# Kernel optimization log

Hardware: AMD Instinct MI355X
Metric: run time of the kernel (lower is better)

Reference implementation:

```python
import jax, jax.numpy as jnp
import numpy as np

SIG_LEVEL = 2
N_UNITS = 1024
INPUT_SIZE = 512
SIGSIZE = sum(2 ** k for k in range(1, SIG_LEVEL + 1))  # siglength(2, L) = 2^(L+1)-2 = 6
SAVED_LEN = N_UNITS * (1 + SIGSIZE)  # 7168
BATCH = 4096


def sigjoin(prev_sigs, disp, time_lapse, level):
    """Chen's identity: new_sig = prev_sig (tensor-mult) exp(v), truncated at `level`.

    prev_sigs: [N, SIGSIZE] flat signature levels (level k occupies 2^k entries),
    disp: [N, 1] displacement in dim 0; dim 1 displacement fixed to time_lapse.
    """
    N = prev_sigs.shape[0]
    v = jnp.concatenate([disp, jnp.full_like(disp, 1.0) * time_lapse], axis=1)  # [N, 2]
    # signature of the straight segment: seg_k = v^{(x)k} / k!
    seg = [v]
    for k in range(2, level + 1):
        seg.append((seg[-1][:, :, None] * v[:, None, :]).reshape(N, -1) / k)
    # split prev signature into levels
    S, off = [], 0
    for k in range(1, level + 1):
        sz = 2 ** k
        S.append(prev_sigs[:, off:off + sz])
        off += sz
    # result_k = S_k + seg_k + sum_{i=1}^{k-1} S_i (x) seg_{k-i}
    out = []
    for k in range(1, level + 1):
        r = S[k - 1] + seg[k - 1]
        for i in range(1, k):
            r = r + (S[i - 1][:, :, None] * seg[k - i - 1][:, None, :]).reshape(N, 2 ** k)
        out.append(r)
    return jnp.concatenate(out, axis=1)


def setup_inputs() -> dict:
    key = jax.random.key(0)
    ks = jax.random.split(key, 8)
    x = jax.random.normal(ks[0], (BATCH, INPUT_SIZE), dtype=jnp.float32)
    prev_sigs = jax.random.normal(ks[1], (BATCH, N_UNITS * SIGSIZE), dtype=jnp.float32) * 0.1
    prev_states = jax.random.normal(ks[2], (BATCH, N_UNITS), dtype=jnp.float32)
    W_w = jax.random.normal(ks[3], (N_UNITS, INPUT_SIZE), dtype=jnp.float32) / np.sqrt(INPUT_SIZE)
    W_b = jax.random.normal(ks[4], (N_UNITS,), dtype=jnp.float32) * 0.01
    U_w = jax.random.normal(ks[5], (N_UNITS, SAVED_LEN), dtype=jnp.float32) / np.sqrt(SAVED_LEN)
    U_b = jax.random.normal(ks[6], (N_UNITS,), dtype=jnp.float32) * 0.01
    log_timelapse = jnp.array([np.log(0.1)], dtype=jnp.float32)
    return {"x": x, "prev_sigs": prev_sigs, "prev_states": prev_states,
            "W_w": W_w, "W_b": W_b, "U_w": U_w, "U_b": U_b,
            "log_timelapse": log_timelapse}


def reference(x, prev_sigs, prev_states, W_w, W_b, U_w, U_b, log_timelapse):
    h = x @ W_w.T + W_b                                  # [B, n_units]
    mem = jnp.concatenate([prev_sigs, prev_states], 1)   # [B, saved_len]
    raw = h + mem @ U_w.T + U_b                          # [B, n_units]
    disp = (raw - prev_states).reshape(-1, 1)            # [B*n_units, 1]
    tl = jnp.exp(log_timelapse)[0]
    sigs = sigjoin(prev_sigs.reshape(-1, SIGSIZE), disp, tl, SIG_LEVEL)
    sigs = sigs.reshape(-1, N_UNITS * SIGSIZE)
    # output_signatures=True: output = [sigs, raw_output]
    return jnp.concatenate([sigs, raw], axis=1)          # [B, n_units*(sigsize+1)]
```

## Files before the change

kernel.cpp:

```cpp
#include <hip/hip_runtime.h>
#include <hip/hip_bf16.h>
#include <cmath>

#define BATCH   4096
#define NUNITS  1024
#define INSIZE  512
#define SIGSZ   6
#define KSIG    (NUNITS * SIGSZ)
#define SAVED   (KSIG + NUNITS)
#define KTOT    (INSIZE + KSIG + NUNITS)
#define OUTW    (NUNITS * (SIGSZ + 1))
#define NKT     (KTOT / 64)

#define WS_AX 0LL
#define WS_AS 2097152LL
#define WS_AT 27262976LL
#define WS_BW 31457280LL
#define WS_BU 31981568LL
#define WS_ELEMS 39321600LL
#define WS_BYTES (WS_ELEMS * 2)

typedef __attribute__((ext_vector_type(8))) short bf16x8;
typedef __attribute__((ext_vector_type(8))) unsigned short u16x8;
typedef __attribute__((ext_vector_type(4))) float f32x4;

__device__ __forceinline__ unsigned short f2bf(float f) {
    union { float f; unsigned int u; } c; c.f = f;
    unsigned int u = c.u;
    return (unsigned short)((u + 0x7FFFu + ((u >> 16) & 1u)) >> 16);
}
__device__ __forceinline__ float bf2f(unsigned short h) {
    union { unsigned int u; float f; } c; c.u = ((unsigned int)h) << 16;
    return c.f;
}

__device__ __forceinline__ int swz(int row, int bytecol) {
    return row * 64 + (((bytecol) ^ ((row & 7) << 4)) >> 1);
}

__global__ __launch_bounds__(256)
void prepack(const float* __restrict__ x, const float* __restrict__ sigs,
             const float* __restrict__ states, const float* __restrict__ Ww,
             const float* __restrict__ Uw, unsigned short* __restrict__ ws)
{
    const long long stride = (long long)gridDim.x * blockDim.x;
    for (long long p = (long long)blockIdx.x * blockDim.x + threadIdx.x;
         p < 4915200LL; p += stride) {
        const float* src; unsigned short* dst; long long o;
        if (p < 262144LL)       { src = x;      dst = ws + WS_AX; o = p; }
        else if (p < 3407872LL) { src = sigs;   dst = ws + WS_AS; o = p - 262144LL; }
        else if (p < 3932160LL) { src = states; dst = ws + WS_AT; o = p - 3407872LL; }
        else if (p < 3997696LL) { src = Ww;     dst = ws + WS_BW; o = p - 3932160LL; }
        else                    { src = Uw;     dst = ws + WS_BU; o = p - 3997696LL; }
        const f32x4 v0 = __builtin_nontemporal_load((const f32x4*)(src + o * 8));
        const f32x4 v1 = __builtin_nontemporal_load((const f32x4*)(src + o * 8) + 1);
        u16x8 h;
        h[0] = f2bf(v0[0]); h[1] = f2bf(v0[1]); h[2] = f2bf(v0[2]); h[3] = f2bf(v0[3]);
        h[4] = f2bf(v1[0]); h[5] = f2bf(v1[1]); h[6] = f2bf(v1[2]); h[7] = f2bf(v1[3]);
        *(u16x8*)(dst + o * 8) = h;
    }
}

#define GLD_LDS(G, L) __builtin_amdgcn_global_load_lds(                        \
        (const __attribute__((address_space(1))) unsigned int*)(G),           \
        (__attribute__((address_space(3))) unsigned int*)(L), 16, 0, 0)

__global__ __launch_bounds__(1024, 1)
void rsig_gemm(const unsigned short* __restrict__ ws,
               const float* __restrict__ Wb,
               const float* __restrict__ Ub,
               const float* __restrict__ lt,
               float* __restrict__ out)
{
    __shared__ unsigned short lds[3 * 16384 + 16384];

    const int t  = threadIdx.x;
    const int bn = blockIdx.x & 7;
    const int bm = blockIdx.x >> 3;

    const int lane = t & 63;
    const int w    = t >> 6;
    const int wm   = w >> 3;
    const int wn   = (w >> 1) & 3;
    const int wk   = w & 1;
    const int lr   = lane & 15;
    const int lg   = lane >> 4;

    const unsigned short* wsAx = ws + WS_AX;
    const unsigned short* wsAs = ws + WS_AS;
    const unsigned short* wsAt = ws + WS_AT;
    const unsigned short* wsBw = ws + WS_BW;
    const unsigned short* wsBu = ws + WS_BU;

    unsigned short* stash = &lds[3 * 16384];
    const int kt0 = 104 + bn * 2;

    const int sRow = lane >> 3;
    const int sCol = 8 * ((lane & 7) ^ sRow);
    const int arow = bm * 128 + w * 8 + sRow;
    const int brow = bn * 128 + w * 8 + sRow;

    f32x4 acc[4][2];
#pragma unroll
    for (int m = 0; m < 4; ++m)
#pragma unroll
        for (int n = 0; n < 2; ++n)
            acc[m][n] = (f32x4)0.f;

    {
        const unsigned short* ga = wsAx + (size_t)arow * INSIZE + sCol;
        const unsigned short* gb = wsBw + (size_t)brow * INSIZE + sCol;
        GLD_LDS(ga,       &lds[0 * 16384 + w * 512]);
        GLD_LDS(gb,       &lds[0 * 16384 + 8192 + w * 512]);
        GLD_LDS(ga + 64,  &lds[1 * 16384 + w * 512]);
        GLD_LDS(gb + 64,  &lds[1 * 16384 + 8192 + w * 512]);
    }

    const unsigned short* saPtr = wsAx + (size_t)arow * INSIZE + 128 + sCol;
    const unsigned short* sbPtr = wsBw + (size_t)brow * INSIZE + 128 + sCol;

    int cur = 0;
    for (int kt = 0; kt < NKT; ++kt) {
        if (kt < NKT - 1) { asm volatile("s_waitcnt vmcnt(2)" ::: "memory"); }
        else              { asm volatile("s_waitcnt vmcnt(0)" ::: "memory"); }
        __builtin_amdgcn_s_barrier();
        __builtin_amdgcn_sched_barrier(0);

        const int st = kt + 2;
        if (st < NKT) {
            if (st == 8) {
                saPtr = wsAs + (size_t)arow * KSIG  + sCol;
                sbPtr = wsBu + (size_t)brow * SAVED + sCol;
            } else if (st == 104) {
                saPtr = wsAt + (size_t)arow * NUNITS + sCol;
            }
            int nb = cur + 2; if (nb >= 3) nb -= 3;
            unsigned short* base = &lds[nb * 16384];
            GLD_LDS(saPtr, base + w * 512);
            GLD_LDS(sbPtr, base + 8192 + w * 512);
            saPtr += 64;
            sbPtr += 64;
        }

        if (kt == kt0) {
            const u16x8 v = *(const u16x8*)&lds[cur * 16384 + t * 8];
            *(u16x8*)&stash[t * 8] = v;
        } else if (kt == kt0 + 1) {
            const u16x8 v = *(const u16x8*)&lds[cur * 16384 + t * 8];
            *(u16x8*)&stash[8192 + t * 8] = v;
        }

        {
            const unsigned short* aT = &lds[cur * 16384];
            const unsigned short* bT = aT + 8192;
            bf16x8 af[4], bfr[2];
#pragma unroll
            for (int m = 0; m < 4; ++m)
                af[m] = *(const bf16x8*)&aT[swz(wm * 64 + m * 16 + lr, wk * 64 + lg * 16)];
#pragma unroll
            for (int n = 0; n < 2; ++n)
                bfr[n] = *(const bf16x8*)&bT[swz(wn * 32 + n * 16 + lr, wk * 64 + lg * 16)];
            __builtin_amdgcn_s_setprio(1);
#pragma unroll
            for (int m = 0; m < 4; ++m)
#pragma unroll
                for (int n = 0; n < 2; ++n)
                    acc[m][n] = __builtin_amdgcn_mfma_f32_16x16x32_bf16(af[m], bfr[n], acc[m][n], 0, 0, 0);
            __builtin_amdgcn_s_setprio(0);
        }

        cur = (cur == 2) ? 0 : cur + 1;
    }

    __syncthreads();

    float* rawt = (float*)lds;
    if (wk == 0) {
#pragma unroll
        for (int n = 0; n < 2; ++n) {
            const int cc = wn * 32 + n * 16 + lr;
            const int ug = bn * 128 + cc;
            const float bias = Wb[ug] + Ub[ug];
#pragma unroll
            for (int m = 0; m < 4; ++m) {
                const int rr = wm * 64 + m * 16 + lg * 4;
#pragma unroll
                for (int i = 0; i < 4; ++i)
                    rawt[(rr + i) * 132 + cc] = acc[m][n][i] + bias;
            }
        }
    }
    __syncthreads();
    if (wk == 1) {
#pragma unroll
        for (int n = 0; n < 2; ++n) {
            const int cc = wn * 32 + n * 16 + lr;
#pragma unroll
            for (int m = 0; m < 4; ++m) {
                const int rr = wm * 64 + m * 16 + lg * 4;
#pragma unroll
                for (int i = 0; i < 4; ++i)
                    rawt[(rr + i) * 132 + cc] += acc[m][n][i];
            }
        }
    }
    __syncthreads();

    const float tl = expf(lt[0]);
    const int r0 = t >> 8;
    const int c  = t & 255;

#define PS(R, CC) bf2f(stash[((CC) >> 6) * 8192 + ((R) >> 3) * 512 + ((R) & 7) * 64 \
                            + (((((CC) & 63) >> 3) ^ ((R) & 7)) << 3) + ((CC) & 7)])

    for (int pass = 0; pass < 32; ++pass) {
        const int r = pass * 4 + r0;
        const long long b = (long long)bm * 128 + r;
        if (c < 192) {
            const int u  = (2 * c) / 3;
            const int cs = c % 3;
            const unsigned short* srow = wsAs + b * KSIG + bn * 768;
            const ushort4 sin = *(const ushort4*)(srow + c * 4);
            const float e0 = bf2f(sin.x), e1 = bf2f(sin.y);
            const float e2 = bf2f(sin.z), e3 = bf2f(sin.w);
            float4 o;
            if (cs == 0) {
                const float d = rawt[r * 132 + u] - PS(r, u);
                o.x = e0 + d;
                o.y = e1 + tl;
                o.z = e2 + d  * (0.5f * d  + e0);
                o.w = e3 + tl * (0.5f * d  + e0);
            } else if (cs == 1) {
                const float d  = rawt[r * 132 + u]     - PS(r, u);
                const float dn = rawt[r * 132 + u + 1] - PS(r, u + 1);
                const float s1 = bf2f(srow[u * 6 + 1]);
                o.x = e0 + d  * (0.5f * tl + s1);
                o.y = e1 + tl * (0.5f * tl + s1);
                o.z = e2 + dn;
                o.w = e3 + tl;
            } else {
                const float d = rawt[r * 132 + u] - PS(r, u);
                const unsigned int sv = *(const unsigned int*)(srow + u * 6);
                const float s0 = bf2f((unsigned short)(sv & 0xffffu));
                const float s1 = bf2f((unsigned short)(sv >> 16));
                o.x = e0 + d  * (0.5f * d  + s0);
                o.y = e1 + tl * (0.5f * d  + s0);
                o.z = e2 + d  * (0.5f * tl + s1);
                o.w = e3 + tl * (0.5f * tl + s1);
            }
            *(float4*)(out + b * OUTW + bn * 768 + c * 4) = o;
        } else if (c < 224) {
            const int cc = (c - 192) * 4;
            const float4 rv = *(const float4*)&rawt[r * 132 + cc];
            *(float4*)(out + b * OUTW + KSIG + bn * 128 + cc) = rv;
        }
    }
#undef PS
}

extern "C" void kernel_launch(void* const* d_in, const int* in_sizes, int n_in,
                              void* d_out, int out_size, void* d_ws, size_t ws_size,
                              hipStream_t stream) {
    const float* x      = (const float*)d_in[0];
    const float* sigs   = (const float*)d_in[1];
    const float* states = (const float*)d_in[2];
    const float* Ww     = (const float*)d_in[3];
    const float* Wb     = (const float*)d_in[4];
    const float* Uw     = (const float*)d_in[5];
    const float* Ub     = (const float*)d_in[6];
    const float* lt     = (const float*)d_in[7];
    float* out = (float*)d_out;

    unsigned short* ws = (unsigned short*)d_ws;
    hipLaunchKernelGGL(prepack, dim3(2048), dim3(256), 0, stream,
                       x, sigs, states, Ww, Uw, ws);
    hipLaunchKernelGGL(rsig_gemm, dim3(256), dim3(1024), 0, stream,
                       ws, Wb, Ub, lt, out);
}
```

Before: 147.5 us.

## Switch GEMM to 32x32x16 MFMA with four-way K split across waves

Replaces the 16x16x32 bf16 MFMA tiling with 32x32x16 MFMA, re-partitioning the 16 waves into 2 M by 2 N by 4 K groups with 64x64 per-wave tiles. This is meant to cut LDS fragment reads per MFMA and raise MFMA efficiency. The cost is a four-stage serialized split-K reduction through LDS with extra barriers in the epilogue. The s_setprio hints are also dropped.

```diff
diff --git a/kernel.cpp b/kernel.cpp
--- a/kernel.cpp
+++ b/kernel.cpp
@@ -20,9 +20,10 @@
 #define WS_ELEMS 39321600LL
 #define WS_BYTES (WS_ELEMS * 2)
 
-typedef __attribute__((ext_vector_type(8))) short bf16x8;
-typedef __attribute__((ext_vector_type(8))) unsigned short u16x8;
-typedef __attribute__((ext_vector_type(4))) float f32x4;
+typedef __attribute__((ext_vector_type(8)))  short bf16x8;
+typedef __attribute__((ext_vector_type(8)))  unsigned short u16x8;
+typedef __attribute__((ext_vector_type(4)))  float f32x4;
+typedef __attribute__((ext_vector_type(16))) float f32x16;
 
 __device__ __forceinline__ unsigned short f2bf(float f) {
     union { float f; unsigned int u; } c; c.f = f;
@@ -81,10 +82,11 @@
     const int lane = t & 63;
     const int w    = t >> 6;
     const int wm   = w >> 3;
-    const int wn   = (w >> 1) & 3;
-    const int wk   = w & 1;
-    const int lr   = lane & 15;
-    const int lg   = lane >> 4;
+    const int wn   = (w >> 2) & 1;
+    const int wk   = w & 3;
+    const int l31  = lane & 31;
+    const int lkh  = lane >> 5;
+    const int rcol = wk * 32 + lkh * 16;
 
     const unsigned short* wsAx = ws + WS_AX;
     const unsigned short* wsAs = ws + WS_AS;
@@ -100,12 +102,12 @@
     const int arow = bm * 128 + w * 8 + sRow;
     const int brow = bn * 128 + w * 8 + sRow;
 
-    f32x4 acc[4][2];
-#pragma unroll
-    for (int m = 0; m < 4; ++m)
+    f32x16 acc[2][2];
+#pragma unroll
+    for (int m = 0; m < 2; ++m)
 #pragma unroll
         for (int n = 0; n < 2; ++n)
-            acc[m][n] = (f32x4)0.f;
+            acc[m][n] = (f32x16)0.f;
 
     {
         const unsigned short* ga = wsAx + (size_t)arow * INSIZE + sCol;
@@ -153,20 +155,19 @@
         {
             const unsigned short* aT = &lds[cur * 16384];
             const unsigned short* bT = aT + 8192;
-            bf16x8 af[4], bfr[2];
-#pragma unroll
-            for (int m = 0; m < 4; ++m)
-                af[m] = *(const bf16x8*)&aT[swz(wm * 64 + m * 16 + lr, wk * 64 + lg * 16)];
+            bf16x8 af[2], bfr[2];
+#pragma unroll
+            for (int m = 0; m < 2; ++m)
+                af[m] = *(const bf16x8*)&aT[swz(wm * 64 + m * 32 + l31, rcol)];
 #pragma unroll
             for (int n = 0; n < 2; ++n)
-                bfr[n] = *(const bf16x8*)&bT[swz(wn * 32 + n * 16 + lr, wk * 64 + lg * 16)];
-            __builtin_amdgcn_s_setprio(1);
-#pragma unroll
-            for (int m = 0; m < 4; ++m)
+                bfr[n] = *(const bf16x8*)&bT[swz(wn * 64 + n * 32 + l31, rcol)];
+#pragma unroll
+            for (int m = 0; m < 2; ++m)
 #pragma unroll
                 for (int n = 0; n < 2; ++n)
-                    acc[m][n] = __builtin_amdgcn_mfma_f32_16x16x32_bf16(af[m], bfr[n], acc[m][n], 0, 0, 0);
-            __builtin_amdgcn_s_setprio(0);
+                    acc[m][n] = __builtin_amdgcn_mfma_f32_32x32x16_bf16(
+                        af[m], bfr[n], acc[m][n], 0, 0, 0);
         }
 
         cur = (cur == 2) ? 0 : cur + 1;
@@ -175,36 +176,41 @@
     __syncthreads();
 
     float* rawt = (float*)lds;
+    const int rowoff = 4 * lkh;
     if (wk == 0) {
 #pragma unroll
-        for (int n = 0; n < 2; ++n) {
-            const int cc = wn * 32 + n * 16 + lr;
-            const int ug = bn * 128 + cc;
-            const float bias = Wb[ug] + Ub[ug];
-#pragma unroll
-            for (int m = 0; m < 4; ++m) {
-                const int rr = wm * 64 + m * 16 + lg * 4;
-#pragma unroll
-                for (int i = 0; i < 4; ++i)
-                    rawt[(rr + i) * 132 + cc] = acc[m][n][i] + bias;
+        for (int m = 0; m < 2; ++m)
+#pragma unroll
+            for (int n = 0; n < 2; ++n) {
+                const int cc = wn * 64 + n * 32 + l31;
+                const int rr = wm * 64 + m * 32 + rowoff;
+                const float bias = Wb[bn * 128 + cc] + Ub[bn * 128 + cc];
+#pragma unroll
+                for (int reg = 0; reg < 16; ++reg) {
+                    const int r = rr + (reg & 3) + 8 * (reg >> 2);
+                    rawt[r * 132 + cc] = acc[m][n][reg] + bias;
+                }
             }
-        }
     }
     __syncthreads();
-    if (wk == 1) {
-#pragma unroll
-        for (int n = 0; n < 2; ++n) {
-            const int cc = wn * 32 + n * 16 + lr;
-#pragma unroll
-            for (int m = 0; m < 4; ++m) {
-                const int rr = wm * 64 + m * 16 + lg * 4;
-#pragma unroll
-                for (int i = 0; i < 4; ++i)
-                    rawt[(rr + i) * 132 + cc] += acc[m][n][i];
-            }
-        }
-    }
-    __syncthreads();
+#pragma unroll
+    for (int slot = 1; slot < 4; ++slot) {
+        if (wk == slot) {
+#pragma unroll
+            for (int m = 0; m < 2; ++m)
+#pragma unroll
+                for (int n = 0; n < 2; ++n) {
+                    const int cc = wn * 64 + n * 32 + l31;
+                    const int rr = wm * 64 + m * 32 + rowoff;
+#pragma unroll
+                    for (int reg = 0; reg < 16; ++reg) {
+                        const int r = rr + (reg & 3) + 8 * (reg >> 2);
+                        rawt[r * 132 + cc] += acc[m][n][reg];
+                    }
+                }
+        }
+        __syncthreads();
+    }
 
     const float tl = expf(lt[0]);
     const int r0 = t >> 8;
```

Result: slower. 150.7 us (+2.1%).
